# Optimization experiments

Measured on AMD Instinct MI355X. Metric: run time of the kernel, lower is better.

Reference implementation:

```python
import jax, jax.numpy as jnp
import numpy as np

N_NODES = 50000
N_EDGES = 800000
IN_CH, HID, HEADS, OUT_CH = 16, 64, 4, 8
NEG_SLOPE = 0.2


def _add_self_loops(edge_index, num_nodes):
    loop = jnp.arange(num_nodes, dtype=edge_index.dtype)
    loops = jnp.stack([loop, loop])  # [2, N]
    return jnp.concatenate([edge_index, loops], axis=1)


def _gat_conv(x, src, dst, W, a_src, a_dst, bias, concat):
    """PyG-style GATConv: linear -> per-edge LeakyReLU attention -> segment
    softmax over incoming edges -> scatter-add aggregate."""
    N = x.shape[0]
    H, C = a_src.shape
    h = (x @ W).reshape(N, H, C)                      # [N,H,C]
    alpha_src = (h * a_src).sum(-1)                   # [N,H]
    alpha_dst = (h * a_dst).sum(-1)                   # [N,H]
    e = jax.nn.leaky_relu(alpha_src[src] + alpha_dst[dst], NEG_SLOPE)  # [E,H]
    # numerically stable segment softmax over edges grouped by dst
    e_max = jax.ops.segment_max(e, dst, num_segments=N)
    e_exp = jnp.exp(e - e_max[dst])
    denom = jax.ops.segment_sum(e_exp, dst, num_segments=N)
    alpha = e_exp / denom[dst]                        # [E,H]
    msg = h[src] * alpha[:, :, None]                  # [E,H,C]
    out = jax.ops.segment_sum(msg, dst, num_segments=N)  # [N,H,C]
    if concat:
        return out.reshape(N, H * C) + bias
    return out.mean(axis=1) + bias


def setup_inputs() -> dict:
    key = jax.random.key(0)
    ks = jax.random.split(key, 12)
    s = 0.1
    return {
        "x": jax.random.normal(ks[0], (N_NODES, IN_CH), jnp.float32),
        "edge_index": jax.random.randint(ks[1], (2, N_EDGES), 0, N_NODES, jnp.int64),
        "W1": jax.random.normal(ks[2], (IN_CH, HEADS * HID), jnp.float32) * s,
        "as1": jax.random.normal(ks[3], (HEADS, HID), jnp.float32) * s,
        "ad1": jax.random.normal(ks[4], (HEADS, HID), jnp.float32) * s,
        "b1": jnp.zeros((HEADS * HID,), jnp.float32),
        "W2": jax.random.normal(ks[5], (HEADS * HID, HEADS * HID), jnp.float32) * s,
        "as2": jax.random.normal(ks[6], (HEADS, HID), jnp.float32) * s,
        "ad2": jax.random.normal(ks[7], (HEADS, HID), jnp.float32) * s,
        "b2": jnp.zeros((HID,), jnp.float32),
        "Wc": jax.random.normal(ks[8], (HID, OUT_CH), jnp.float32) * s,
        "bc": jnp.zeros((OUT_CH,), jnp.float32),
    }


def reference(x, edge_index, W1, as1, ad1, b1, W2, as2, ad2, b2, Wc, bc):
    ei = _add_self_loops(edge_index, x.shape[0])
    src, dst = ei[0], ei[1]
    h = _gat_conv(x, src, dst, W1, as1, ad1, b1, concat=True)
    h = jax.nn.elu(h)
    h = _gat_conv(h, src, dst, W2, as2, ad2, b2, concat=False)
    h = jax.nn.elu(h)
    return h @ Wc + bc  # [N, OUT_CH]
```

## Files before the change

kernel.cpp:

```cpp
#include <hip/hip_runtime.h>
#include <math.h>

#define NODES   50000
#define HEADS   4
#define HID     64
#define FDIM    256
#define IN_CH   16
#define NEG_SLOPE 0.2f

typedef unsigned short ushort_t;
typedef unsigned int uint_t;
typedef __attribute__((ext_vector_type(8))) short bf16x8;
typedef __attribute__((ext_vector_type(4))) float f32x4;
typedef __attribute__((ext_vector_type(4))) uint_t u32x4;

__device__ inline ushort_t f2bf(float f) {
    uint_t u = __float_as_uint(f);
    u += 0x7fffu + ((u >> 16) & 1u);
    return (ushort_t)(u >> 16);
}
__device__ inline uint_t f2h(float f) {
    _Float16 h = (_Float16)f;
    return (uint_t)*(ushort_t*)&h;
}
__device__ inline float h2f(uint_t u) {
    ushort_t us = (ushort_t)u;
    _Float16 h = *(_Float16*)&us;
    return (float)h;
}

__device__ inline void fmamix8(float* a, uint4 hv, float pw) {
    asm("v_fma_mix_f32 %0, %8, %9, %0 op_sel:[0,0,0] op_sel_hi:[0,1,0]\n\t"
        "v_fma_mix_f32 %1, %8, %9, %1 op_sel:[0,1,0] op_sel_hi:[0,1,0]\n\t"
        "v_fma_mix_f32 %2, %8, %10, %2 op_sel:[0,0,0] op_sel_hi:[0,1,0]\n\t"
        "v_fma_mix_f32 %3, %8, %10, %3 op_sel:[0,1,0] op_sel_hi:[0,1,0]\n\t"
        "v_fma_mix_f32 %4, %8, %11, %4 op_sel:[0,0,0] op_sel_hi:[0,1,0]\n\t"
        "v_fma_mix_f32 %5, %8, %11, %5 op_sel:[0,1,0] op_sel_hi:[0,1,0]\n\t"
        "v_fma_mix_f32 %6, %8, %12, %6 op_sel:[0,0,0] op_sel_hi:[0,1,0]\n\t"
        "v_fma_mix_f32 %7, %8, %12, %7 op_sel:[0,1,0] op_sel_hi:[0,1,0]"
        : "+v"(a[0]), "+v"(a[1]), "+v"(a[2]), "+v"(a[3]),
          "+v"(a[4]), "+v"(a[5]), "+v"(a[6]), "+v"(a[7])
        : "v"(pw), "v"(hv.x), "v"(hv.y), "v"(hv.z), "v"(hv.w));
}


__global__ __launch_bounds__(256) void k_prep(const float* __restrict__ x,
                                              const float* __restrict__ W1,
                                              const float* __restrict__ as1,
                                              const float* __restrict__ ad1,
                                              const float* __restrict__ W2,
                                              const int* __restrict__ ei, int E,
                                              ushort_t* __restrict__ h,
                                              float* __restrict__ asrc,
                                              float* __restrict__ adst,
                                              ushort_t* __restrict__ W2T,
                                              int* __restrict__ deg, int Nn, int NB) {
    int bid = blockIdx.x, t = threadIdx.x;
    if (bid >= NB + 256) {
        int e = (bid - NB - 256) * 256 + t;
        int Etot = E + Nn;
        if (e >= Etot) return;
        int d = (e < E) ? ei[E + e] : (e - E);
        if (d >= 0 && d < Nn) atomicAdd(&deg[d], 1);
        return;
    }
    if (bid >= NB) {
        int idx = (bid - NB) * 256 + t;
        int n = idx >> 8, k = idx & 255;
        W2T[idx] = f2bf(W2[k * FDIM + n]);
        return;
    }
    float w1c[16];
#pragma unroll
    for (int k = 0; k < 16; ++k) w1c[k] = W1[k * FDIM + t];
    float av = as1[t], dv = ad1[t];
    int hh = t >> 6;
#pragma unroll
    for (int j = 0; j < 8; ++j) {
        int n = bid * 8 + j;
        if (n >= Nn) break;
        const float4* xp = (const float4*)(x + n * IN_CH);
        float4 x0 = xp[0], x1 = xp[1], x2 = xp[2], x3 = xp[3];
        float s = x0.x * w1c[0]  + x0.y * w1c[1]  + x0.z * w1c[2]  + x0.w * w1c[3]
                + x1.x * w1c[4]  + x1.y * w1c[5]  + x1.z * w1c[6]  + x1.w * w1c[7]
                + x2.x * w1c[8]  + x2.y * w1c[9]  + x2.z * w1c[10] + x2.w * w1c[11]
                + x3.x * w1c[12] + x3.y * w1c[13] + x3.z * w1c[14] + x3.w * w1c[15];
        uint_t pv = f2h(s);
        uint_t ov = __shfl_down(pv, 1);
        if (!(t & 1))
            *(uint_t*)(h + (((long)hh * Nn + n) << 6) + (t & 63)) = pv | (ov << 16);
        float p1 = s * av, p2 = s * dv;
#pragma unroll
        for (int off = 1; off < 64; off <<= 1) {
            p1 += __shfl_xor(p1, off);
            p2 += __shfl_xor(p2, off);
        }
        if ((t & 63) == 0) {
            asrc[n * 4 + hh] = p1;
            adst[n * 4 + hh] = p2;
        }
    }
}


__global__ __launch_bounds__(256) void k_scanA(const int* __restrict__ deg,
                                               int* __restrict__ bsum, int N) {
    __shared__ int sh[256];
    int t = threadIdx.x;
    int i0 = blockIdx.x * 4096 + t * 16;
    int s = 0;
#pragma unroll
    for (int j = 0; j < 16; ++j) s += (i0 + j < N) ? deg[i0 + j] : 0;
    sh[t] = s;
    __syncthreads();
    for (int off = 128; off; off >>= 1) {
        if (t < off) sh[t] += sh[t + off];
        __syncthreads();
    }
    if (t == 0) bsum[blockIdx.x] = sh[0];
}

__global__ void k_scanB(int* __restrict__ bsum, int* __restrict__ rowst, int nb, int N) {
    int t = threadIdx.x;
    int orig = (t < nb) ? bsum[t] : 0;
    int v = orig;
#pragma unroll
    for (int off = 1; off < 64; off <<= 1) {
        int u = __shfl_up(v, off);
        if (t >= off) v += u;
    }
    if (t < nb) bsum[t] = v - orig;
    if (t == 63) rowst[N] = v;
}

__global__ __launch_bounds__(256) void k_scanC(const int* __restrict__ deg,
                                               const int* __restrict__ bsum,
                                               int* __restrict__ rowst,
                                               int* __restrict__ cursor, int N) {
    __shared__ int sh[256];
    int t = threadIdx.x, b = blockIdx.x;
    int i0 = b * 4096 + t * 16;
    int v[16], s = 0;
#pragma unroll
    for (int j = 0; j < 16; ++j) { v[j] = (i0 + j < N) ? deg[i0 + j] : 0; s += v[j]; }
    sh[t] = s;
    __syncthreads();
    for (int off = 1; off < 256; off <<= 1) {
        int u = (t >= off) ? sh[t - off] : 0;
        __syncthreads();
        sh[t] += u;
        __syncthreads();
    }
    int excl = sh[t] - s + bsum[b];
#pragma unroll
    for (int j = 0; j < 16; ++j) {
        if (i0 + j < N) { rowst[i0 + j] = excl; cursor[i0 + j] = excl; }
        excl += v[j];
    }
}

__global__ void k_scatter(const int* __restrict__ ei, int E, int N,
                          int* __restrict__ cursor, int2* __restrict__ csr2) {
    int e = blockIdx.x * blockDim.x + threadIdx.x;
    int Etot = E + N;
    if (e >= Etot) return;
    int s, d;
    if (e < E) { s = ei[e]; d = ei[E + e]; } else { s = d = e - E; }
    if (d < 0 || d >= N) return;
    int pos = atomicAdd(&cursor[d], 1);
    csr2[pos] = make_int2(s, d);
}


__global__ __launch_bounds__(256) void k_gemm2(const ushort_t* __restrict__ A,
                                               const ushort_t* __restrict__ BT,
                                               const float* __restrict__ as2,
                                               const float* __restrict__ ad2,
                                               ushort_t* __restrict__ C,
                                               float* __restrict__ asrc,
                                               float* __restrict__ adst, int M) {
    __shared__ short As[64 * 40];
    __shared__ short Bs[64 * 40];
    __shared__ float2 red[64][2];
    int tid = threadIdx.x;
    int row0 = blockIdx.y * 64, col0 = blockIdx.x * 64;
    int wid = tid >> 6, lane = tid & 63;
    int wm = wid >> 1, wn = wid & 1;
    int quad = lane >> 4, lm = lane & 15;
    int lr = tid >> 2, lk = (tid & 3) * 8;
    f32x4 acc[2][2] = {};
    for (int k0 = 0; k0 < FDIM; k0 += 32) {
        uint4 av = {0u, 0u, 0u, 0u};
        int ar = row0 + lr;
        if (ar < M) av = *(const uint4*)(A + (long)ar * FDIM + k0 + lk);
        *(uint4*)(&As[lr * 40 + lk]) = av;
        uint4 bv = *(const uint4*)(BT + (long)(col0 + lr) * FDIM + k0 + lk);
        *(uint4*)(&Bs[lr * 40 + lk]) = bv;
        __syncthreads();
        bf16x8 a0 = *(const bf16x8*)(&As[(wm * 32 + lm) * 40 + quad * 8]);
        bf16x8 a1 = *(const bf16x8*)(&As[(wm * 32 + 16 + lm) * 40 + quad * 8]);
        bf16x8 b0 = *(const bf16x8*)(&Bs[(wn * 32 + lm) * 40 + quad * 8]);
        bf16x8 b1 = *(const bf16x8*)(&Bs[(wn * 32 + 16 + lm) * 40 + quad * 8]);
        acc[0][0] = __builtin_amdgcn_mfma_f32_16x16x32_bf16(a0, b0, acc[0][0], 0, 0, 0);
        acc[0][1] = __builtin_amdgcn_mfma_f32_16x16x32_bf16(a0, b1, acc[0][1], 0, 0, 0);
        acc[1][0] = __builtin_amdgcn_mfma_f32_16x16x32_bf16(a1, b0, acc[1][0], 0, 0, 0);
        acc[1][1] = __builtin_amdgcn_mfma_f32_16x16x32_bf16(a1, b1, acc[1][1], 0, 0, 0);
        __syncthreads();
    }
#pragma unroll
    for (int mi = 0; mi < 2; ++mi)
#pragma unroll
        for (int ni = 0; ni < 2; ++ni)
#pragma unroll
            for (int r = 0; r < 4; ++r) {
                int row = row0 + wm * 32 + mi * 16 + quad * 4 + r;
                int colw = wn * 32 + ni * 16 + lm;
                if (row < M)
                    C[(((long)blockIdx.x * M + row) << 6) + colw] = (ushort_t)f2h(acc[mi][ni][r]);
            }
    float asv0 = as2[col0 + wn * 32 + lm], asv1 = as2[col0 + wn * 32 + 16 + lm];
    float adv0 = ad2[col0 + wn * 32 + lm], adv1 = ad2[col0 + wn * 32 + 16 + lm];
#pragma unroll
    for (int mi = 0; mi < 2; ++mi)
#pragma unroll
        for (int r = 0; r < 4; ++r) {
            float ps = acc[mi][0][r] * asv0 + acc[mi][1][r] * asv1;
            float pd = acc[mi][0][r] * adv0 + acc[mi][1][r] * adv1;
#pragma unroll
            for (int off = 1; off < 16; off <<= 1) {
                ps += __shfl_xor(ps, off);
                pd += __shfl_xor(pd, off);
            }
            if (lm == 0) red[wm * 32 + mi * 16 + quad * 4 + r][wn] = make_float2(ps, pd);
        }
    __syncthreads();
    if (tid < 64) {
        int row = row0 + tid;
        if (row < M) {
            float2 e0 = red[tid][0], e1 = red[tid][1];
            asrc[row * 4 + blockIdx.x] = e0.x + e1.x;
            adst[row * 4 + blockIdx.x] = e0.y + e1.y;
        }
    }
}


__global__ void k_pw(const int2* __restrict__ csr2, const float* __restrict__ asrc,
                     const float* __restrict__ adst, uint_t* __restrict__ pwb, int Etot) {
    int e = blockIdx.x * blockDim.x + threadIdx.x;
    if (e >= Etot) return;
    int2 sd = csr2[e];
    float4 av = *(const float4*)(asrc + sd.x * 4);
    float4 dv = *(const float4*)(adst + sd.y * 4);
    float t[4] = {av.x + dv.x, av.y + dv.y, av.z + dv.z, av.w + dv.w};
    uint_t sh = (uint_t)sd.x << 16;
#pragma unroll
    for (int h = 0; h < 4; ++h) {
        float tt = (t[h] > 0.f) ? t[h] : NEG_SLOPE * t[h];
        pwb[h * Etot + e] = sh | f2h(__expf(tt));
    }
}


__global__ __launch_bounds__(256) void k_agg(const ushort_t* __restrict__ h,
                                             const uint_t* __restrict__ pwb,
                                             const int* __restrict__ row_start,
                                             const float* __restrict__ b1,
                                             ushort_t* __restrict__ hout,
                                             ushort_t* __restrict__ zn,
                                             int mode, int Etot, int N) {
    int tid  = threadIdx.x;
    int bid  = blockIdx.x;
    int head = bid & 3;
    int nb   = bid >> 2;
    int wv   = tid >> 6;
    int lane = tid & 63;
    int half = lane >> 5;
    int l32  = lane & 31;
    int g    = l32 >> 3;
    int cg   = l32 & 7;
    int d    = nb * 8 + wv * 2 + half;
    bool valid = d < N;

    int s0 = 0, s1 = 0;
    if (valid) { s0 = row_start[d]; s1 = row_start[d + 1]; }
    int cnt  = s1 - s0;
    int maxc = max(cnt, __shfl_xor(cnt, 32));

    const char* hb  = (const char*)h + ((size_t)head * (size_t)N << 7);
    const char* pwc = (const char*)pwb;
    uint_t loff  = (uint_t)cg * 16;
    uint_t pbyte = ((uint_t)head * (uint_t)Etot + (uint_t)(s0 + g)) << 2;

    float acc[8] = {0.f, 0.f, 0.f, 0.f, 0.f, 0.f, 0.f, 0.f};
    float den = 0.f;

    for (int off = 0; off < maxc; off += 16) {
        int i0 = s0 + off + g;
        uint_t pb = pbyte + ((uint_t)off << 2);
        uint_t u0 = (i0      < s1) ? __builtin_nontemporal_load((const uint_t*)(pwc + pb))      : 0u;
        uint_t u1 = (i0 + 4  < s1) ? __builtin_nontemporal_load((const uint_t*)(pwc + pb + 16)) : 0u;
        uint_t u2 = (i0 + 8  < s1) ? __builtin_nontemporal_load((const uint_t*)(pwc + pb + 32)) : 0u;
        uint_t u3 = (i0 + 12 < s1) ? __builtin_nontemporal_load((const uint_t*)(pwc + pb + 48)) : 0u;
        uint4 hv0 = *(const uint4*)(hb + (((u0 >> 16) << 7) + loff));
        uint4 hv1 = *(const uint4*)(hb + (((u1 >> 16) << 7) + loff));
        uint4 hv2 = *(const uint4*)(hb + (((u2 >> 16) << 7) + loff));
        uint4 hv3 = *(const uint4*)(hb + (((u3 >> 16) << 7) + loff));
        float pw0 = h2f(u0), pw1 = h2f(u1);
        float pw2 = h2f(u2), pw3 = h2f(u3);
        den += (pw0 + pw1) + (pw2 + pw3);
        fmamix8(acc, hv0, pw0);
        fmamix8(acc, hv1, pw1);
        fmamix8(acc, hv2, pw2);
        fmamix8(acc, hv3, pw3);
    }
#pragma unroll
    for (int off = 8; off <= 16; off <<= 1) {
#pragma unroll
        for (int j = 0; j < 8; ++j) acc[j] += __shfl_xor(acc[j], off);
        den += __shfl_xor(den, off);
    }

    if (g != 0 || !valid) return;
    float inv = 1.f / den;
    if (mode) {
        const float* bp = b1 + head * HID + cg * 8;
        float v[8];
#pragma unroll
        for (int j = 0; j < 8; ++j) {
            float t = acc[j] * inv + bp[j];
            v[j] = (t > 0.f) ? t : __expf(t) - 1.f;
        }
        u32x4 u;
        u.x = (uint_t)f2bf(v[0]) | ((uint_t)f2bf(v[1]) << 16);
        u.y = (uint_t)f2bf(v[2]) | ((uint_t)f2bf(v[3]) << 16);
        u.z = (uint_t)f2bf(v[4]) | ((uint_t)f2bf(v[5]) << 16);
        u.w = (uint_t)f2bf(v[6]) | ((uint_t)f2bf(v[7]) << 16);
        __builtin_nontemporal_store(u, (u32x4*)(hout + (long)d * FDIM + head * HID + cg * 8));
    } else {
        u32x4 u;
        u.x = f2h(acc[0] * inv) | (f2h(acc[1] * inv) << 16);
        u.y = f2h(acc[2] * inv) | (f2h(acc[3] * inv) << 16);
        u.z = f2h(acc[4] * inv) | (f2h(acc[5] * inv) << 16);
        u.w = f2h(acc[6] * inv) | (f2h(acc[7] * inv) << 16);
        __builtin_nontemporal_store(u, (u32x4*)(zn + (((long)head * N + d) << 6) + cg * 8));
    }
}


__global__ __launch_bounds__(256) void k_fin(const ushort_t* __restrict__ zn,
                                             const float* __restrict__ b2,
                                             const float* __restrict__ Wc,
                                             const float* __restrict__ bc,
                                             float* __restrict__ out, int N) {
    __shared__ float zsh[256];
    __shared__ float wsh[584];
    int tid = threadIdx.x;
    for (int i = tid; i < 584; i += 256)
        wsh[i] = (i < 512) ? Wc[i] : ((i < 520) ? bc[i - 512] : b2[i - 520]);
    __syncthreads();
    int ln = tid >> 6, c = tid & 63;
    int n = blockIdx.x * 4 + ln;
    if (n < N) {
        long base = ((long)n << 6) + c;
        long hs = (long)N << 6;
        float v = 0.25f * (h2f(zn[base]) + h2f(zn[base + hs])
                         + h2f(zn[base + 2 * hs]) + h2f(zn[base + 3 * hs]))
                + wsh[520 + c];
        zsh[ln * 64 + c] = (v > 0.f) ? v : __expf(v) - 1.f;
    }
    __syncthreads();
    if (tid < 32) {
        int ln2 = tid >> 3, o = tid & 7;
        int nn = blockIdx.x * 4 + ln2;
        if (nn < N) {
            float acc = wsh[512 + o];
            const float* zp = zsh + ln2 * 64;
#pragma unroll 8
            for (int c2 = 0; c2 < 64; ++c2) acc += zp[c2] * wsh[c2 * 8 + o];
            out[(long)nn * 8 + o] = acc;
        }
    }
}


extern "C" void kernel_launch(void* const* d_in, const int* in_sizes, int n_in,
                              void* d_out, int out_size, void* d_ws, size_t ws_size,
                              hipStream_t stream) {
    const float* x   = (const float*)d_in[0];
    const int*   ei  = (const int*)d_in[1];
    const float* W1  = (const float*)d_in[2];
    const float* as1 = (const float*)d_in[3];
    const float* ad1 = (const float*)d_in[4];
    const float* b1  = (const float*)d_in[5];
    const float* W2  = (const float*)d_in[6];
    const float* as2 = (const float*)d_in[7];
    const float* ad2 = (const float*)d_in[8];
    const float* b2  = (const float*)d_in[9];
    const float* Wc  = (const float*)d_in[10];
    const float* bc  = (const float*)d_in[11];
    float* out = (float*)d_out;

    const int N = NODES;
    const int E = in_sizes[1] / 2;
    const int Etot = E + N;

    char* ws = (char*)d_ws;
    size_t off = 0;
    auto alloc = [&](size_t bytes) {
        void* p = ws + off;
        off = (off + bytes + 255) & ~(size_t)255;
        return p;
    };
    ushort_t* hbf    = (ushort_t*)alloc((size_t)N * FDIM * 2);
    ushort_t* hact   = (ushort_t*)alloc((size_t)N * FDIM * 2);
    float*    asrc   = (float*)alloc((size_t)N * HEADS * 4);
    float*    adst   = (float*)alloc((size_t)N * HEADS * 4);
    ushort_t* W2T    = (ushort_t*)alloc((size_t)FDIM * FDIM * 2);
    int*      deg    = (int*)alloc((size_t)N * 4);
    int*      rowst  = (int*)alloc((size_t)(N + 1) * 4);
    int*      cursor = (int*)alloc((size_t)N * 4);
    int*      bsum   = (int*)alloc(64 * 4);
    int2*     csr2   = (int2*)alloc((size_t)Etot * 8);
    uint_t*   pwb    = (uint_t*)alloc((size_t)Etot * HEADS * 4);
    ushort_t* znorm  = hact;

    const int tpb = 256;
    int egrid = (Etot + tpb - 1) / tpb;
    int nb = (N + 4095) / 4096;
    int NB = (N + 7) / 8;
    int agrid = 4 * ((N + 7) / 8);

    hipMemsetAsync(deg, 0, (size_t)N * 4, stream);

    k_prep<<<NB + 256 + egrid, tpb, 0, stream>>>(x, W1, as1, ad1, W2, ei, E,
                                                 hbf, asrc, adst, W2T, deg, N, NB);
    k_scanA<<<nb, 256, 0, stream>>>(deg, bsum, N);
    k_scanB<<<1, 64, 0, stream>>>(bsum, rowst, nb, N);
    k_scanC<<<nb, 256, 0, stream>>>(deg, bsum, rowst, cursor, N);
    k_scatter<<<egrid, tpb, 0, stream>>>(ei, E, N, cursor, csr2);

    k_pw<<<egrid, tpb, 0, stream>>>(csr2, asrc, adst, pwb, Etot);
    k_agg<<<agrid, 256, 0, stream>>>(hbf, pwb, rowst, b1, hact, nullptr, 1, Etot, N);

    dim3 g2(FDIM / 64, (N + 63) / 64);
    k_gemm2<<<g2, 256, 0, stream>>>(hact, W2T, as2, ad2, hbf, asrc, adst, N);
    k_pw<<<egrid, tpb, 0, stream>>>(csr2, asrc, adst, pwb, Etot);
    k_agg<<<agrid, 256, 0, stream>>>(hbf, pwb, rowst, nullptr, nullptr, znorm, 0, Etot, N);
    k_fin<<<(N + 3) / 4, 256, 0, stream>>>(znorm, b2, Wc, bc, out, N);
}
```

Measured before the change: 374.1 us.

## Fuse edge attention weight computation into aggregation and store only CSR sources

```diff
diff --git a/kernel.cpp b/kernel.cpp
--- a/kernel.cpp
+++ b/kernel.cpp
@@ -78,7 +78,6 @@
 #pragma unroll
     for (int j = 0; j < 8; ++j) {
         int n = bid * 8 + j;
-        if (n >= Nn) break;
         const float4* xp = (const float4*)(x + n * IN_CH);
         float4 x0 = xp[0], x1 = xp[1], x2 = xp[2], x3 = xp[3];
         float s = x0.x * w1c[0]  + x0.y * w1c[1]  + x0.z * w1c[2]  + x0.w * w1c[3]
@@ -160,7 +159,7 @@
 }
 
 __global__ void k_scatter(const int* __restrict__ ei, int E, int N,
-                          int* __restrict__ cursor, int2* __restrict__ csr2) {
+                          int* __restrict__ cursor, int* __restrict__ csrc) {
     int e = blockIdx.x * blockDim.x + threadIdx.x;
     int Etot = E + N;
     if (e >= Etot) return;
@@ -168,7 +167,7 @@
     if (e < E) { s = ei[e]; d = ei[E + e]; } else { s = d = e - E; }
     if (d < 0 || d >= N) return;
     int pos = atomicAdd(&cursor[d], 1);
-    csr2[pos] = make_int2(s, d);
+    csrc[pos] = s;
 }
 
 
@@ -245,30 +244,15 @@
 }
 
 
-__global__ void k_pw(const int2* __restrict__ csr2, const float* __restrict__ asrc,
-                     const float* __restrict__ adst, uint_t* __restrict__ pwb, int Etot) {
-    int e = blockIdx.x * blockDim.x + threadIdx.x;
-    if (e >= Etot) return;
-    int2 sd = csr2[e];
-    float4 av = *(const float4*)(asrc + sd.x * 4);
-    float4 dv = *(const float4*)(adst + sd.y * 4);
-    float t[4] = {av.x + dv.x, av.y + dv.y, av.z + dv.z, av.w + dv.w};
-    uint_t sh = (uint_t)sd.x << 16;
-#pragma unroll
-    for (int h = 0; h < 4; ++h) {
-        float tt = (t[h] > 0.f) ? t[h] : NEG_SLOPE * t[h];
-        pwb[h * Etot + e] = sh | f2h(__expf(tt));
-    }
-}
-
-
 __global__ __launch_bounds__(256) void k_agg(const ushort_t* __restrict__ h,
-                                             const uint_t* __restrict__ pwb,
+                                             const int* __restrict__ csrc,
                                              const int* __restrict__ row_start,
+                                             const float* __restrict__ asrc,
+                                             const float* __restrict__ adst,
                                              const float* __restrict__ b1,
                                              ushort_t* __restrict__ hout,
                                              ushort_t* __restrict__ zn,
-                                             int mode, int Etot, int N) {
+                                             int mode, int N) {
     int tid  = threadIdx.x;
     int bid  = blockIdx.x;
     int head = bid & 3;
@@ -287,27 +271,38 @@
     int cnt  = s1 - s0;
     int maxc = max(cnt, __shfl_xor(cnt, 32));
 
-    const char* hb  = (const char*)h + ((size_t)head * (size_t)N << 7);
-    const char* pwc = (const char*)pwb;
-    uint_t loff  = (uint_t)cg * 16;
-    uint_t pbyte = ((uint_t)head * (uint_t)Etot + (uint_t)(s0 + g)) << 2;
+    const char* hb = (const char*)h + ((size_t)head * (size_t)N << 7);
+    uint_t loff = (uint_t)cg * 16;
+    const float* asp = asrc + head;
+    float adv = valid ? adst[d * 4 + head] : 0.f;
 
     float acc[8] = {0.f, 0.f, 0.f, 0.f, 0.f, 0.f, 0.f, 0.f};
     float den = 0.f;
 
     for (int off = 0; off < maxc; off += 16) {
         int i0 = s0 + off + g;
-        uint_t pb = pbyte + ((uint_t)off << 2);
-        uint_t u0 = (i0      < s1) ? __builtin_nontemporal_load((const uint_t*)(pwc + pb))      : 0u;
-        uint_t u1 = (i0 + 4  < s1) ? __builtin_nontemporal_load((const uint_t*)(pwc + pb + 16)) : 0u;
-        uint_t u2 = (i0 + 8  < s1) ? __builtin_nontemporal_load((const uint_t*)(pwc + pb + 32)) : 0u;
-        uint_t u3 = (i0 + 12 < s1) ? __builtin_nontemporal_load((const uint_t*)(pwc + pb + 48)) : 0u;
-        uint4 hv0 = *(const uint4*)(hb + (((u0 >> 16) << 7) + loff));
-        uint4 hv1 = *(const uint4*)(hb + (((u1 >> 16) << 7) + loff));
-        uint4 hv2 = *(const uint4*)(hb + (((u2 >> 16) << 7) + loff));
-        uint4 hv3 = *(const uint4*)(hb + (((u3 >> 16) << 7) + loff));
-        float pw0 = h2f(u0), pw1 = h2f(u1);
-        float pw2 = h2f(u2), pw3 = h2f(u3);
+        int t0 = (i0      < s1) ? __builtin_nontemporal_load(csrc + i0)      : -1;
+        int t1 = (i0 + 4  < s1) ? __builtin_nontemporal_load(csrc + i0 + 4)  : -1;
+        int t2 = (i0 + 8  < s1) ? __builtin_nontemporal_load(csrc + i0 + 8)  : -1;
+        int t3 = (i0 + 12 < s1) ? __builtin_nontemporal_load(csrc + i0 + 12) : -1;
+        uint_t u0 = (t0 < 0) ? 0u : (uint_t)t0;
+        uint_t u1 = (t1 < 0) ? 0u : (uint_t)t1;
+        uint_t u2 = (t2 < 0) ? 0u : (uint_t)t2;
+        uint_t u3 = (t3 < 0) ? 0u : (uint_t)t3;
+        uint4 hv0 = *(const uint4*)(hb + ((u0 << 7) + loff));
+        uint4 hv1 = *(const uint4*)(hb + ((u1 << 7) + loff));
+        uint4 hv2 = *(const uint4*)(hb + ((u2 << 7) + loff));
+        uint4 hv3 = *(const uint4*)(hb + ((u3 << 7) + loff));
+        float q0 = asp[u0 * 4], q1 = asp[u1 * 4];
+        float q2 = asp[u2 * 4], q3 = asp[u3 * 4];
+        float w0 = q0 + adv; w0 = (w0 > 0.f) ? w0 : NEG_SLOPE * w0;
+        float w1 = q1 + adv; w1 = (w1 > 0.f) ? w1 : NEG_SLOPE * w1;
+        float w2 = q2 + adv; w2 = (w2 > 0.f) ? w2 : NEG_SLOPE * w2;
+        float w3 = q3 + adv; w3 = (w3 > 0.f) ? w3 : NEG_SLOPE * w3;
+        float pw0 = (t0 >= 0) ? __expf(w0) : 0.f;
+        float pw1 = (t1 >= 0) ? __expf(w1) : 0.f;
+        float pw2 = (t2 >= 0) ? __expf(w2) : 0.f;
+        float pw3 = (t3 >= 0) ? __expf(w3) : 0.f;
         den += (pw0 + pw1) + (pw2 + pw3);
         fmamix8(acc, hv0, pw0);
         fmamix8(acc, hv1, pw1);
@@ -421,8 +416,7 @@
     int*      rowst  = (int*)alloc((size_t)(N + 1) * 4);
     int*      cursor = (int*)alloc((size_t)N * 4);
     int*      bsum   = (int*)alloc(64 * 4);
-    int2*     csr2   = (int2*)alloc((size_t)Etot * 8);
-    uint_t*   pwb    = (uint_t*)alloc((size_t)Etot * HEADS * 4);
+    int*      csrc   = (int*)alloc((size_t)Etot * 4);
     ushort_t* znorm  = hact;
 
     const int tpb = 256;
@@ -438,14 +432,14 @@
     k_scanA<<<nb, 256, 0, stream>>>(deg, bsum, N);
     k_scanB<<<1, 64, 0, stream>>>(bsum, rowst, nb, N);
     k_scanC<<<nb, 256, 0, stream>>>(deg, bsum, rowst, cursor, N);
-    k_scatter<<<egrid, tpb, 0, stream>>>(ei, E, N, cursor, csr2);
-
-    k_pw<<<egrid, tpb, 0, stream>>>(csr2, asrc, adst, pwb, Etot);
-    k_agg<<<agrid, 256, 0, stream>>>(hbf, pwb, rowst, b1, hact, nullptr, 1, Etot, N);
+    k_scatter<<<egrid, tpb, 0, stream>>>(ei, E, N, cursor, csrc);
+
+    k_agg<<<agrid, 256, 0, stream>>>(hbf, csrc, rowst, asrc, adst, b1,
+                                     hact, nullptr, 1, N);
 
     dim3 g2(FDIM / 64, (N + 63) / 64);
     k_gemm2<<<g2, 256, 0, stream>>>(hact, W2T, as2, ad2, hbf, asrc, adst, N);
-    k_pw<<<egrid, tpb, 0, stream>>>(csr2, asrc, adst, pwb, Etot);
-    k_agg<<<agrid, 256, 0, stream>>>(hbf, pwb, rowst, nullptr, nullptr, znorm, 0, Etot, N);
+    k_agg<<<agrid, 256, 0, stream>>>(hbf, csrc, rowst, asrc, adst, nullptr,
+                                     nullptr, znorm, 0, N);
     k_fin<<<(N + 3) / 4, 256, 0, stream>>>(znorm, b2, Wc, bc, out, N);
 }
```

Result: slower. 409.7 us (+9.5%).

## Split per-head features into 32-channel slices for finer-grained gather aggregation

Applied to the files above, without the earlier changes.

```diff
diff --git a/kernel.cpp b/kernel.cpp
--- a/kernel.cpp
+++ b/kernel.cpp
@@ -75,10 +75,10 @@
     for (int k = 0; k < 16; ++k) w1c[k] = W1[k * FDIM + t];
     float av = as1[t], dv = ad1[t];
     int hh = t >> 6;
+    int sl = t >> 5;
 #pragma unroll
     for (int j = 0; j < 8; ++j) {
         int n = bid * 8 + j;
-        if (n >= Nn) break;
         const float4* xp = (const float4*)(x + n * IN_CH);
         float4 x0 = xp[0], x1 = xp[1], x2 = xp[2], x3 = xp[3];
         float s = x0.x * w1c[0]  + x0.y * w1c[1]  + x0.z * w1c[2]  + x0.w * w1c[3]
@@ -88,7 +88,7 @@
         uint_t pv = f2h(s);
         uint_t ov = __shfl_down(pv, 1);
         if (!(t & 1))
-            *(uint_t*)(h + (((long)hh * Nn + n) << 6) + (t & 63)) = pv | (ov << 16);
+            *(uint_t*)(h + (((long)sl * Nn + n) << 5) + (t & 31)) = pv | (ov << 16);
         float p1 = s * av, p2 = s * dv;
 #pragma unroll
         for (int off = 1; off < 64; off <<= 1) {
@@ -216,7 +216,8 @@
                 int row = row0 + wm * 32 + mi * 16 + quad * 4 + r;
                 int colw = wn * 32 + ni * 16 + lm;
                 if (row < M)
-                    C[(((long)blockIdx.x * M + row) << 6) + colw] = (ushort_t)f2h(acc[mi][ni][r]);
+                    C[(((long)(blockIdx.x * 2 + (colw >> 5)) * M + row) << 5) + (colw & 31)]
+                        = (ushort_t)f2h(acc[mi][ni][r]);
             }
     float asv0 = as2[col0 + wn * 32 + lm], asv1 = as2[col0 + wn * 32 + 16 + lm];
     float adv0 = ad2[col0 + wn * 32 + lm], adv1 = ad2[col0 + wn * 32 + 16 + lm];
@@ -271,14 +272,15 @@
                                              int mode, int Etot, int N) {
     int tid  = threadIdx.x;
     int bid  = blockIdx.x;
-    int head = bid & 3;
-    int nb   = bid >> 2;
+    int sl   = bid & 7;
+    int head = sl >> 1;
+    int nb   = bid >> 3;
     int wv   = tid >> 6;
     int lane = tid & 63;
     int half = lane >> 5;
     int l32  = lane & 31;
-    int g    = l32 >> 3;
-    int cg   = l32 & 7;
+    int g    = l32 >> 2;
+    int cg   = l32 & 3;
     int d    = nb * 8 + wv * 2 + half;
     bool valid = d < N;
 
@@ -287,7 +289,7 @@
     int cnt  = s1 - s0;
     int maxc = max(cnt, __shfl_xor(cnt, 32));
 
-    const char* hb  = (const char*)h + ((size_t)head * (size_t)N << 7);
+    const char* hb  = (const char*)h + ((size_t)sl * (size_t)N << 6);
     const char* pwc = (const char*)pwb;
     uint_t loff  = (uint_t)cg * 16;
     uint_t pbyte = ((uint_t)head * (uint_t)Etot + (uint_t)(s0 + g)) << 2;
@@ -295,19 +297,19 @@
     float acc[8] = {0.f, 0.f, 0.f, 0.f, 0.f, 0.f, 0.f, 0.f};
     float den = 0.f;
 
-    for (int off = 0; off < maxc; off += 16) {
+    for (int off = 0; off < maxc; off += 32) {
         int i0 = s0 + off + g;
         uint_t pb = pbyte + ((uint_t)off << 2);
         uint_t u0 = (i0      < s1) ? __builtin_nontemporal_load((const uint_t*)(pwc + pb))      : 0u;
-        uint_t u1 = (i0 + 4  < s1) ? __builtin_nontemporal_load((const uint_t*)(pwc + pb + 16)) : 0u;
-        uint_t u2 = (i0 + 8  < s1) ? __builtin_nontemporal_load((const uint_t*)(pwc + pb + 32)) : 0u;
-        uint_t u3 = (i0 + 12 < s1) ? __builtin_nontemporal_load((const uint_t*)(pwc + pb + 48)) : 0u;
-        uint4 hv0 = *(const uint4*)(hb + (((u0 >> 16) << 7) + loff));
-        uint4 hv1 = *(const uint4*)(hb + (((u1 >> 16) << 7) + loff));
-        uint4 hv2 = *(const uint4*)(hb + (((u2 >> 16) << 7) + loff));
-        uint4 hv3 = *(const uint4*)(hb + (((u3 >> 16) << 7) + loff));
-        float pw0 = h2f(u0), pw1 = h2f(u1);
-        float pw2 = h2f(u2), pw3 = h2f(u3);
+        uint_t u1 = (i0 + 8  < s1) ? __builtin_nontemporal_load((const uint_t*)(pwc + pb + 32)) : 0u;
+        uint_t u2 = (i0 + 16 < s1) ? __builtin_nontemporal_load((const uint_t*)(pwc + pb + 64)) : 0u;
+        uint_t u3 = (i0 + 24 < s1) ? __builtin_nontemporal_load((const uint_t*)(pwc + pb + 96)) : 0u;
+        uint4 hv0 = *(const uint4*)(hb + (((u0 >> 16) << 6) + loff));
+        uint4 hv1 = *(const uint4*)(hb + (((u1 >> 16) << 6) + loff));
+        uint4 hv2 = *(const uint4*)(hb + (((u2 >> 16) << 6) + loff));
+        uint4 hv3 = *(const uint4*)(hb + (((u3 >> 16) << 6) + loff));
+        float pw0 = h2f(u0 & 0xffffu), pw1 = h2f(u1 & 0xffffu);
+        float pw2 = h2f(u2 & 0xffffu), pw3 = h2f(u3 & 0xffffu);
         den += (pw0 + pw1) + (pw2 + pw3);
         fmamix8(acc, hv0, pw0);
         fmamix8(acc, hv1, pw1);
@@ -315,7 +317,7 @@
         fmamix8(acc, hv3, pw3);
     }
 #pragma unroll
-    for (int off = 8; off <= 16; off <<= 1) {
+    for (int off = 4; off <= 16; off <<= 1) {
 #pragma unroll
         for (int j = 0; j < 8; ++j) acc[j] += __shfl_xor(acc[j], off);
         den += __shfl_xor(den, off);
@@ -324,7 +326,7 @@
     if (g != 0 || !valid) return;
     float inv = 1.f / den;
     if (mode) {
-        const float* bp = b1 + head * HID + cg * 8;
+        const float* bp = b1 + sl * 32 + cg * 8;
         float v[8];
 #pragma unroll
         for (int j = 0; j < 8; ++j) {
@@ -336,14 +338,14 @@
         u.y = (uint_t)f2bf(v[2]) | ((uint_t)f2bf(v[3]) << 16);
         u.z = (uint_t)f2bf(v[4]) | ((uint_t)f2bf(v[5]) << 16);
         u.w = (uint_t)f2bf(v[6]) | ((uint_t)f2bf(v[7]) << 16);
-        __builtin_nontemporal_store(u, (u32x4*)(hout + (long)d * FDIM + head * HID + cg * 8));
+        __builtin_nontemporal_store(u, (u32x4*)(hout + (long)d * FDIM + sl * 32 + cg * 8));
     } else {
         u32x4 u;
         u.x = f2h(acc[0] * inv) | (f2h(acc[1] * inv) << 16);
         u.y = f2h(acc[2] * inv) | (f2h(acc[3] * inv) << 16);
         u.z = f2h(acc[4] * inv) | (f2h(acc[5] * inv) << 16);
         u.w = f2h(acc[6] * inv) | (f2h(acc[7] * inv) << 16);
-        __builtin_nontemporal_store(u, (u32x4*)(zn + (((long)head * N + d) << 6) + cg * 8));
+        __builtin_nontemporal_store(u, (u32x4*)(zn + (((long)sl * N + d) << 5) + cg * 8));
     }
 }
 
@@ -362,10 +364,11 @@
     int ln = tid >> 6, c = tid & 63;
     int n = blockIdx.x * 4 + ln;
     if (n < N) {
-        long base = ((long)n << 6) + c;
-        long hs = (long)N << 6;
-        float v = 0.25f * (h2f(zn[base]) + h2f(zn[base + hs])
-                         + h2f(zn[base + 2 * hs]) + h2f(zn[base + 3 * hs]))
+        int chh = c >> 5, c32 = c & 31;
+        long hs2 = (long)N << 5;
+        long base = ((long)chh * N << 5) + ((long)n << 5) + c32;
+        float v = 0.25f * (h2f(zn[base]) + h2f(zn[base + 2 * hs2])
+                         + h2f(zn[base + 4 * hs2]) + h2f(zn[base + 6 * hs2]))
                 + wsh[520 + c];
         zsh[ln * 64 + c] = (v > 0.f) ? v : __expf(v) - 1.f;
     }
@@ -429,7 +432,7 @@
     int egrid = (Etot + tpb - 1) / tpb;
     int nb = (N + 4095) / 4096;
     int NB = (N + 7) / 8;
-    int agrid = 4 * ((N + 7) / 8);
+    int agrid = 8 * ((N + 7) / 8);
 
     hipMemsetAsync(deg, 0, (size_t)N * 4, stream);
 
```

New measurement: 432.7 us. 15.7% more time.
